# Kernel tuning notes

Hardware: AMD Instinct MI355X
Metric: run time of the kernel (lower is better)

Reference implementation:

```python
import jax, jax.numpy as jnp
import numpy as np

N_STEPS = 2
MAX_STEP = 1.0
EPS64 = float(np.finfo(np.float64).eps)


def _sphere_log(p, q):
    # log map on unit sphere, tangent at p pointing to q; p,q: [..., D]
    cos = jnp.clip(jnp.sum(p * q, axis=-1, keepdims=True), -1.0, 1.0)
    u = q - cos * p
    un = jnp.linalg.norm(u, axis=-1, keepdims=True)
    theta = jnp.arccos(cos)
    return theta * u / (un + 1e-12)


def _sphere_exp(p, v):
    # exp map on unit sphere; jnp.sinc(n/pi) = sin(n)/n (stable at 0)
    n = jnp.linalg.norm(v, axis=-1, keepdims=True)
    x = jnp.cos(n) * p + jnp.sinc(n / jnp.pi) * v
    return x / jnp.linalg.norm(x, axis=-1, keepdims=True)


def setup_inputs() -> dict:
    key = jax.random.key(0)
    ks = jax.random.split(key, 6)
    N, C, D, E = 50000, 16, 3, 1600000
    nodes = jax.random.normal(ks[0], (N, C, D), dtype=jnp.float32)
    nodes = nodes / jnp.linalg.norm(nodes, axis=-1, keepdims=True)  # points on S^2
    edge_w = jax.random.uniform(ks[1], (E,), dtype=jnp.float32)
    senders = jax.random.randint(ks[2], (E,), 0, N, dtype=jnp.int32)
    receivers = jax.random.randint(ks[3], (E,), 0, N, dtype=jnp.int32)
    t_sqrt = 1.0 + 0.3 * jax.random.normal(ks[4], (C,), dtype=jnp.float32)
    delta_sqrt = 1.0 + 0.3 * jax.random.normal(ks[5], (C,), dtype=jnp.float32)
    return {"nodes": nodes, "edge_w": edge_w, "t_sqrt": t_sqrt,
            "delta_sqrt": delta_sqrt, "senders": senders, "receivers": receivers}


def reference(nodes, edge_w, t_sqrt, delta_sqrt, senders, receivers):
    N = nodes.shape[0]
    t = (t_sqrt ** 2) / N_STEPS            # per-channel time, split across Euler steps
    delta = delta_sqrt ** 2                 # per-channel min step size
    deg = jax.ops.segment_sum(edge_w, senders, num_segments=N)  # [N]

    def laplace(x):
        # graph Laplacian of manifold-valued signal: weighted mean of log maps, negated
        logs = _sphere_log(x[senders], x[receivers])              # [E, C, D]
        agg = jax.ops.segment_sum(edge_w[:, None, None] * logs, senders, num_segments=N)
        return -agg / (deg[:, None, None] + 1e-12)                # [N, C, D]

    def step(x, _):
        v = laplace(x)
        nrm = jnp.sqrt(jnp.sum(v * v, axis=-1) + EPS64)           # [N, C]
        alp = jax.nn.sigmoid(nrm - delta[None, :])
        scale = jnp.where(nrm * alp <= MAX_STEP, alp, MAX_STEP / nrm)
        v = -(v * scale[..., None]) * t[None, :, None]
        return _sphere_exp(x, v), None

    x, _ = jax.lax.scan(step, nodes, None, length=N_STEPS, unroll=N_STEPS)
    return x
```

## Files before the change

kernel.cpp:

```cpp
#include <hip/hip_runtime.h>
#include <math.h>


constexpr float EPS64F = 2.2204460492503131e-16f;
constexpr float PI_F   = 3.14159265358979323846f;
constexpr int   SR_BITS = 14;
constexpr int   CH_BITS = 15;

typedef int   vi4 __attribute__((ext_vector_type(4)));
typedef float vf4 __attribute__((ext_vector_type(4)));
typedef float vf2 __attribute__((ext_vector_type(2)));


__global__ __launch_bounds__(256) void lhist_kernel(
    const int* __restrict__ snd, unsigned char* __restrict__ pos,
    unsigned char* __restrict__ partial2, int E, int NC) {
  __shared__ int h[1 << SR_BITS];
  int tid = threadIdx.x;
  int c = blockIdx.x, s = blockIdx.y;
  for (int i = tid; i < (1 << SR_BITS); i += 256) h[i] = 0;
  __syncthreads();
  int base = c << CH_BITS;
  int cnt = min(1 << CH_BITS, E - base);
  int s0 = s << SR_BITS;
  const vi4* snd4 = (const vi4*)(snd + base);
  int cnt4 = cnt >> 2;
  for (int i = tid; i < cnt4; i += 256) {
    vi4 sv = snd4[i];
    int e = base + (i << 2);
    int v;
    v = sv.x - s0; if ((unsigned)v < (1u << SR_BITS)) pos[e]     = (unsigned char)atomicAdd(&h[v], 1);
    v = sv.y - s0; if ((unsigned)v < (1u << SR_BITS)) pos[e + 1] = (unsigned char)atomicAdd(&h[v], 1);
    v = sv.z - s0; if ((unsigned)v < (1u << SR_BITS)) pos[e + 2] = (unsigned char)atomicAdd(&h[v], 1);
    v = sv.w - s0; if ((unsigned)v < (1u << SR_BITS)) pos[e + 3] = (unsigned char)atomicAdd(&h[v], 1);
  }
  if (tid == 0) {
    for (int i = cnt4 << 2; i < cnt; ++i) {
      int v = snd[base + i] - s0;
      if ((unsigned)v < (1u << SR_BITS))
        pos[base + i] = (unsigned char)atomicAdd(&h[v], 1);
    }
  }
  __syncthreads();
  unsigned char* dst = partial2 + ((size_t)(s * NC + c) << SR_BITS);
  for (int i = tid; i < (1 << SR_BITS); i += 256)
    dst[i] = (unsigned char)h[i];
}

__global__ __launch_bounds__(1024) void scan1A_kernel(
    const unsigned char* __restrict__ partial2, unsigned char* __restrict__ boffL,
    int* __restrict__ row_start, int* __restrict__ btot, int N, int NC) {
  __shared__ int wsum[16];
  int tid = threadIdx.x;
  int lane = tid & 63, wave = tid >> 6;
  int i = blockIdx.x * 1024 + tid;
  int vpad = 0;
  if (i < N) {
    int s = i >> SR_BITS, lv = i & ((1 << SR_BITS) - 1);
    int run = 0;
    for (int c = 0; c < NC; ++c) {
      int t = partial2[((size_t)(s * NC + c) << SR_BITS) + lv];
      boffL[(size_t)c * N + i] = (unsigned char)run;
      run += t;
    }
    vpad = (run + 15) & ~15;
  }
  int incl = vpad;
  #pragma unroll
  for (int off = 1; off < 64; off <<= 1) {
    int t = __shfl_up(incl, off, 64);
    if (lane >= off) incl += t;
  }
  if (lane == 63) wsum[wave] = incl;
  __syncthreads();
  if (wave == 0 && lane < 16) {
    int wincl = wsum[lane];
    #pragma unroll
    for (int off = 1; off < 16; off <<= 1) {
      int t = __shfl_up(wincl, off, 64);
      if (lane >= off) wincl += t;
    }
    wsum[lane] = wincl;
  }
  __syncthreads();
  int woff = (wave > 0) ? wsum[wave - 1] : 0;
  if (i < N) row_start[i] = woff + incl - vpad;
  if (tid == 0) btot[blockIdx.x] = wsum[15];
}

__global__ __launch_bounds__(256) void scanCD_kernel(
    int* __restrict__ row_start, const int* __restrict__ btot, int N, int nb) {
  __shared__ int bsh[64];
  int tid = threadIdx.x;
  if (tid < 64) {
    int v = (tid < nb) ? btot[tid] : 0;
    int incl = v;
    #pragma unroll
    for (int off = 1; off < 64; off <<= 1) {
      int t = __shfl_up(incl, off, 64);
      if (tid >= off) incl += t;
    }
    bsh[tid] = incl - v;
    if (blockIdx.x == 0 && tid == 63) row_start[N] = incl;
  }
  __syncthreads();
  int i = blockIdx.x * 256 + tid;
  if (i >= N) return;
  row_start[i] = row_start[i] + bsh[i >> 10];
}

__global__ __launch_bounds__(256) void fill_kernel(
    const vi4* __restrict__ snd4, const vi4* __restrict__ rcv4,
    const vf4* __restrict__ ew4, const unsigned char* __restrict__ pos,
    const unsigned char* __restrict__ boffL, const int* __restrict__ row_start,
    long long* __restrict__ pair,
    const int* __restrict__ snd, const int* __restrict__ rcv,
    const float* __restrict__ ew, int N, int E) {
  int tid = threadIdx.x;
  int E4 = E >> 2;
  #pragma unroll
  for (int gg = 0; gg < 2; ++gg) {
    int g = blockIdx.x * 512 + gg * 256 + tid;
    if (g < E4) {
      int e = g << 2;
      const unsigned char* bc = boffL + (size_t)(e >> CH_BITS) * N;
      vi4 s = __builtin_nontemporal_load(&snd4[g]);
      vi4 r = __builtin_nontemporal_load(&rcv4[g]);
      vf4 w = __builtin_nontemporal_load(&ew4[g]);
      unsigned pb = *(const unsigned*)(pos + e);
      int rs0 = row_start[s.x] + bc[s.x];
      int rs1 = row_start[s.y] + bc[s.y];
      int rs2 = row_start[s.z] + bc[s.z];
      int rs3 = row_start[s.w] + bc[s.w];
      pair[rs0 + (pb & 255u)] =
          (long long)(((unsigned long long)(unsigned)__float_as_int(w.x) << 32) | (unsigned)(r.x * 48));
      pair[rs1 + ((pb >> 8) & 255u)] =
          (long long)(((unsigned long long)(unsigned)__float_as_int(w.y) << 32) | (unsigned)(r.y * 48));
      pair[rs2 + ((pb >> 16) & 255u)] =
          (long long)(((unsigned long long)(unsigned)__float_as_int(w.z) << 32) | (unsigned)(r.z * 48));
      pair[rs3 + (pb >> 24)] =
          (long long)(((unsigned long long)(unsigned)__float_as_int(w.w) << 32) | (unsigned)(r.w * 48));
    }
  }
  if (blockIdx.x == 0 && tid == 0) {
    for (int e = E4 << 2; e < E; ++e) {
      int sn = snd[e];
      pair[row_start[sn] + boffL[(size_t)(e >> CH_BITS) * N + sn] + pos[e]] =
          (long long)(((unsigned long long)(unsigned)__float_as_int(ew[e]) << 32) | (unsigned)(rcv[e] * 48));
    }
  }
}


__device__ __forceinline__ void edge_accum_pk(
    vf2 p0, vf2 p1, vf2 p2, vf2 q0, vf2 q1, vf2 q2, vf2 w,
    vf2& a0, vf2& a1, vf2& a2) {
  vf2 cs = p0 * q0 + p1 * q1 + p2 * q2;
  cs = __builtin_elementwise_min(vf2{1.f, 1.f},
       __builtin_elementwise_max(vf2{-1.f, -1.f}, cs));
  vf2 u0 = q0 - cs * p0;
  vf2 u1 = q1 - cs * p1;
  vf2 u2 = q2 - cs * p2;
  vf2 un2 = __builtin_elementwise_max(u0 * u0 + u1 * u1 + u2 * u2,
                                      vf2{1e-24f, 1e-24f});
  vf2 ax = __builtin_elementwise_abs(cs);
  vf2 s = __builtin_elementwise_sqrt(vf2{1.f, 1.f} - ax);
  vf2 poly = ((ax * -0.0187293f + 0.0742610f) * ax - 0.2121144f) * ax
             + 1.5707288f;
  vf2 th = s * poly;
  vf2 theta;
  theta.x = (cs.x >= 0.0f) ? th.x : (PI_F - th.x);
  theta.y = (cs.y >= 0.0f) ? th.y : (PI_F - th.y);
  vf2 rsq;
  rsq.x = __builtin_amdgcn_rsqf(un2.x);
  rsq.y = __builtin_amdgcn_rsqf(un2.y);
  vf2 coef = w * theta * rsq;
  a0 += coef * u0;
  a1 += coef * u1;
  a2 += coef * u2;
}

__device__ __forceinline__ void node_step(
    float a0, float a1, float a2, float ws, float p0, float p1, float p2,
    float ts, float dsv, float& y0, float& y1, float& y2) {
  float invdg = __builtin_amdgcn_rcpf(ws + 1e-12f);
  float g0 = a0 * invdg, g1 = a1 * invdg, g2 = a2 * invdg;
  float nrm = sqrtf(fmaf(g0, g0, fmaf(g1, g1, g2 * g2)) + EPS64F);
  float tch = ts * ts * 0.5f;
  float dch = dsv * dsv;
  float alp = __builtin_amdgcn_rcpf(1.0f + __expf(dch - nrm));
  float scale = (nrm * alp <= 1.0f) ? alp : __builtin_amdgcn_rcpf(nrm);
  float f = scale * tch;
  float v0 = g0 * f, v1 = g1 * f, v2 = g2 * f;
  float nv = sqrtf(fmaf(v0, v0, fmaf(v1, v1, v2 * v2)));
  float cn = __cosf(nv);
  float sc = (nv > 1e-20f) ? (__sinf(nv) * __builtin_amdgcn_rcpf(nv)) : 1.0f;
  float t0 = fmaf(cn, p0, sc * v0);
  float t1 = fmaf(cn, p1, sc * v1);
  float t2 = fmaf(cn, p2, sc * v2);
  float inv = __builtin_amdgcn_rsqf(fmaf(t0, t0, fmaf(t1, t1, t2 * t2)));
  y0 = t0 * inv; y1 = t1 * inv; y2 = t2 * inv;
}

__global__ __launch_bounds__(256, 6) void flowp_kernel(
    const float* __restrict__ xin, const int* __restrict__ row_start,
    const long long* __restrict__ pair, const float* __restrict__ tsq,
    const float* __restrict__ dsq, float* __restrict__ xout, int N) {
  int node = blockIdx.x * 4 + (threadIdx.x >> 6);
  if (node >= N) return;
  int lane = threadIdx.x & 63;
  int c = lane & 15;
  int k = lane >> 4;
  int c3 = c * 3;
  int beg = row_start[node];
  int end = row_start[node + 1];
  int ip = node * 48 + c3;
  float ps0 = xin[ip], ps1 = xin[ip + 1], ps2 = xin[ip + 2];
  vf2 p0 = {ps0, ps0}, p1 = {ps1, ps1}, p2 = {ps2, ps2};
  vf2 a0 = {0.f, 0.f}, a1 = {0.f, 0.f}, a2 = {0.f, 0.f}, wsv = {0.f, 0.f};
  int iters = (end - beg) >> 4;
  if (iters > 0) {
    int j = beg + k;
    long long t0 = __builtin_nontemporal_load(&pair[j]);
    long long t1 = __builtin_nontemporal_load(&pair[j + 4]);
    long long t2 = __builtin_nontemporal_load(&pair[j + 8]);
    long long t3 = __builtin_nontemporal_load(&pair[j + 12]);
    long long eb0 = __builtin_nontemporal_load(&pair[j + 16]);
    long long eb1 = __builtin_nontemporal_load(&pair[j + 20]);
    long long eb2 = __builtin_nontemporal_load(&pair[j + 24]);
    long long eb3 = __builtin_nontemporal_load(&pair[j + 28]);
    float w0 = __int_as_float((int)(t0 >> 32));
    float w1 = __int_as_float((int)(t1 >> 32));
    float w2 = __int_as_float((int)(t2 >> 32));
    float w3 = __int_as_float((int)(t3 >> 32));
    const float* qp;
    qp = xin + ((int)t0 + c3); float qa0 = qp[0], qa1 = qp[1], qa2 = qp[2];
    qp = xin + ((int)t1 + c3); float qb0 = qp[0], qb1 = qp[1], qb2 = qp[2];
    qp = xin + ((int)t2 + c3); float qc0 = qp[0], qc1 = qp[1], qc2 = qp[2];
    qp = xin + ((int)t3 + c3); float qd0 = qp[0], qd1 = qp[1], qd2 = qp[2];
    #pragma unroll 2
    for (int t = 0; t < iters; ++t, j += 16) {
      long long ec0 = __builtin_nontemporal_load(&pair[j + 32]);
      long long ec1 = __builtin_nontemporal_load(&pair[j + 36]);
      long long ec2 = __builtin_nontemporal_load(&pair[j + 40]);
      long long ec3 = __builtin_nontemporal_load(&pair[j + 44]);
      float nw0 = __int_as_float((int)(eb0 >> 32));
      float nw1 = __int_as_float((int)(eb1 >> 32));
      float nw2 = __int_as_float((int)(eb2 >> 32));
      float nw3 = __int_as_float((int)(eb3 >> 32));
      const float* np;
      np = xin + ((int)eb0 + c3); float na0 = np[0], na1 = np[1], na2 = np[2];
      np = xin + ((int)eb1 + c3); float nb0 = np[0], nb1 = np[1], nb2 = np[2];
      np = xin + ((int)eb2 + c3); float nc0 = np[0], nc1 = np[1], nc2 = np[2];
      np = xin + ((int)eb3 + c3); float nd0 = np[0], nd1 = np[1], nd2 = np[2];
      vf2 wA = {w0, w1}, wB = {w2, w3};
      edge_accum_pk(p0, p1, p2, vf2{qa0, qb0}, vf2{qa1, qb1},
                    vf2{qa2, qb2}, wA, a0, a1, a2);
      edge_accum_pk(p0, p1, p2, vf2{qc0, qd0}, vf2{qc1, qd1},
                    vf2{qc2, qd2}, wB, a0, a1, a2);
      wsv += wA + wB;
      w0 = nw0; w1 = nw1; w2 = nw2; w3 = nw3;
      qa0 = na0; qa1 = na1; qa2 = na2;
      qb0 = nb0; qb1 = nb1; qb2 = nb2;
      qc0 = nc0; qc1 = nc1; qc2 = nc2;
      qd0 = nd0; qd1 = nd1; qd2 = nd2;
      eb0 = ec0; eb1 = ec1; eb2 = ec2; eb3 = ec3;
    }
  }
  float A0 = a0.x + a0.y, A1 = a1.x + a1.y, A2 = a2.x + a2.y;
  float ws = wsv.x + wsv.y;
  A0 += __shfl_xor(A0, 16); A1 += __shfl_xor(A1, 16);
  A2 += __shfl_xor(A2, 16); ws += __shfl_xor(ws, 16);
  A0 += __shfl_xor(A0, 32); A1 += __shfl_xor(A1, 32);
  A2 += __shfl_xor(A2, 32); ws += __shfl_xor(ws, 32);
  if (k == 0) {
    float y0, y1, y2;
    node_step(A0, A1, A2, ws, ps0, ps1, ps2, tsq[c], dsq[c], y0, y1, y2);
    xout[ip] = y0; xout[ip + 1] = y1; xout[ip + 2] = y2;
  }
}

static inline size_t al16(size_t x) { return (x + 15) & ~(size_t)15; }

extern "C" void kernel_launch(void* const* d_in, const int* in_sizes, int n_in,
                              void* d_out, int out_size, void* d_ws, size_t ws_size,
                              hipStream_t stream) {
  const float* nodes = (const float*)d_in[0];
  const float* ew    = (const float*)d_in[1];
  const float* tsq   = (const float*)d_in[2];
  const float* dsq   = (const float*)d_in[3];
  const int*   snd   = (const int*)d_in[4];
  const int*   rcv   = (const int*)d_in[5];
  float* out = (float*)d_out;

  int E = in_sizes[1];
  int N = in_sizes[0] / 48;

  int NS = (N + (1 << SR_BITS) - 1) >> SR_BITS;
  int NC = (E + (1 << CH_BITS) - 1) >> CH_BITS;

  size_t padN  = (size_t)E + 15 * (size_t)N + 64;
  size_t rsB   = al16((size_t)(N + 4) * 4);
  size_t auxB  = 512;
  size_t pairB = al16(padN * 8);
  size_t p2B   = al16((size_t)NS * NC << SR_BITS);
  size_t boffB = al16((size_t)NC * N * 4);

  char* base = (char*)d_ws;
  int*           row_start = (int*)base;
  int*           btot      = (int*)(base + rsB);
  long long*     pair      = (long long*)(base + rsB + auxB);
  unsigned char* partial2  = (unsigned char*)(base + rsB + auxB + pairB);
  unsigned char* boffL     = (unsigned char*)(base + rsB + auxB + pairB + p2B);
  unsigned char* pos       = (unsigned char*)(base + rsB + auxB + pairB + p2B + boffB);
  float*         xtmp      = (float*)boffL;

  int E4  = E >> 2;
  int nb  = (N + 1023) / 1024;
  int nb2 = (N + 255) / 256;
  int fbk = (E4 + 511) / 512;
  int nfb = (N + 3) / 4;

  hipMemsetAsync(pair, 0, pairB, stream);
  lhist_kernel<<<dim3(NC, NS), 256, 0, stream>>>(snd, pos, partial2, E, NC);
  scan1A_kernel<<<nb, 1024, 0, stream>>>(partial2, boffL, row_start, btot, N, NC);
  scanCD_kernel<<<nb2, 256, 0, stream>>>(row_start, btot, N, nb);
  fill_kernel<<<fbk, 256, 0, stream>>>((const vi4*)snd, (const vi4*)rcv,
                                       (const vf4*)ew, pos, boffL, row_start,
                                       pair, snd, rcv, ew, N, E);

  flowp_kernel<<<nfb, 256, 0, stream>>>(nodes, row_start, pair, tsq, dsq, xtmp, N);
  flowp_kernel<<<nfb, 256, 0, stream>>>(xtmp, row_start, pair, tsq, dsq, out, N);
}
```

Before: 275.4 us.

## Gather neighbor positions in fp16 and simplify edge loop with higher occupancy

A half-precision copy of the node positions is built inside the scan kernel. Both Euler-step kernels now gather neighbour coordinates from fp16 arrays, and the first step writes its intermediate result in fp16, which halves the bytes of the random gathers that dominate the flow kernels. The centre point for the first step is still read in fp32, but the second step reads its centre from the fp16 intermediate. The hand-written register prefetch pipeline is removed in favour of a plain loop, and the occupancy hint is raised from 6 to 8 to hide latency instead. This trades accuracy (fp16 rounding on the log-map inputs) for less memory traffic.

```diff
diff --git a/kernel.cpp b/kernel.cpp
--- a/kernel.cpp
+++ b/kernel.cpp
@@ -7,9 +7,10 @@
 constexpr int   SR_BITS = 14;
 constexpr int   CH_BITS = 15;
 
-typedef int   vi4 __attribute__((ext_vector_type(4)));
-typedef float vf4 __attribute__((ext_vector_type(4)));
-typedef float vf2 __attribute__((ext_vector_type(2)));
+typedef int      vi4 __attribute__((ext_vector_type(4)));
+typedef float    vf4 __attribute__((ext_vector_type(4)));
+typedef float    vf2 __attribute__((ext_vector_type(2)));
+typedef _Float16 vh4 __attribute__((ext_vector_type(4)));
 
 
 __global__ __launch_bounds__(256) void lhist_kernel(
@@ -89,7 +90,9 @@
 }
 
 __global__ __launch_bounds__(256) void scanCD_kernel(
-    int* __restrict__ row_start, const int* __restrict__ btot, int N, int nb) {
+    int* __restrict__ row_start, const int* __restrict__ btot,
+    const vf4* __restrict__ nodes4, _Float16* __restrict__ nodes_h,
+    int N, int nb) {
   __shared__ int bsh[64];
   int tid = threadIdx.x;
   if (tid < 64) {
@@ -105,8 +108,13 @@
   }
   __syncthreads();
   int i = blockIdx.x * 256 + tid;
-  if (i >= N) return;
-  row_start[i] = row_start[i] + bsh[i >> 10];
+  if (i < N) row_start[i] = row_start[i] + bsh[i >> 10];
+  int total = N * 12;
+  for (int idx = blockIdx.x * 256 + tid; idx < total; idx += gridDim.x * 256) {
+    vf4 v = nodes4[idx];
+    vh4 h = {(_Float16)v.x, (_Float16)v.y, (_Float16)v.z, (_Float16)v.w};
+    ((vh4*)nodes_h)[idx] = h;
+  }
 }
 
 __global__ __launch_bounds__(256) void fill_kernel(
@@ -202,10 +210,11 @@
   y0 = t0 * inv; y1 = t1 * inv; y2 = t2 * inv;
 }
 
-__global__ __launch_bounds__(256, 6) void flowp_kernel(
-    const float* __restrict__ xin, const int* __restrict__ row_start,
-    const long long* __restrict__ pair, const float* __restrict__ tsq,
-    const float* __restrict__ dsq, float* __restrict__ xout, int N) {
+__global__ __launch_bounds__(256, 8) void flowp_kernel(
+    const _Float16* __restrict__ xh, const float* __restrict__ pf,
+    const int* __restrict__ row_start, const long long* __restrict__ pair,
+    const float* __restrict__ tsq, const float* __restrict__ dsq,
+    float* __restrict__ of, _Float16* __restrict__ oh, int N) {
   int node = blockIdx.x * 4 + (threadIdx.x >> 6);
   if (node >= N) return;
   int lane = threadIdx.x & 63;
@@ -215,57 +224,36 @@
   int beg = row_start[node];
   int end = row_start[node + 1];
   int ip = node * 48 + c3;
-  float ps0 = xin[ip], ps1 = xin[ip + 1], ps2 = xin[ip + 2];
+  float ps0, ps1, ps2;
+  if (pf) {
+    ps0 = pf[ip]; ps1 = pf[ip + 1]; ps2 = pf[ip + 2];
+  } else {
+    ps0 = (float)xh[ip]; ps1 = (float)xh[ip + 1]; ps2 = (float)xh[ip + 2];
+  }
   vf2 p0 = {ps0, ps0}, p1 = {ps1, ps1}, p2 = {ps2, ps2};
   vf2 a0 = {0.f, 0.f}, a1 = {0.f, 0.f}, a2 = {0.f, 0.f}, wsv = {0.f, 0.f};
   int iters = (end - beg) >> 4;
-  if (iters > 0) {
-    int j = beg + k;
-    long long t0 = __builtin_nontemporal_load(&pair[j]);
-    long long t1 = __builtin_nontemporal_load(&pair[j + 4]);
-    long long t2 = __builtin_nontemporal_load(&pair[j + 8]);
-    long long t3 = __builtin_nontemporal_load(&pair[j + 12]);
-    long long eb0 = __builtin_nontemporal_load(&pair[j + 16]);
-    long long eb1 = __builtin_nontemporal_load(&pair[j + 20]);
-    long long eb2 = __builtin_nontemporal_load(&pair[j + 24]);
-    long long eb3 = __builtin_nontemporal_load(&pair[j + 28]);
-    float w0 = __int_as_float((int)(t0 >> 32));
-    float w1 = __int_as_float((int)(t1 >> 32));
-    float w2 = __int_as_float((int)(t2 >> 32));
-    float w3 = __int_as_float((int)(t3 >> 32));
-    const float* qp;
-    qp = xin + ((int)t0 + c3); float qa0 = qp[0], qa1 = qp[1], qa2 = qp[2];
-    qp = xin + ((int)t1 + c3); float qb0 = qp[0], qb1 = qp[1], qb2 = qp[2];
-    qp = xin + ((int)t2 + c3); float qc0 = qp[0], qc1 = qp[1], qc2 = qp[2];
-    qp = xin + ((int)t3 + c3); float qd0 = qp[0], qd1 = qp[1], qd2 = qp[2];
-    #pragma unroll 2
-    for (int t = 0; t < iters; ++t, j += 16) {
-      long long ec0 = __builtin_nontemporal_load(&pair[j + 32]);
-      long long ec1 = __builtin_nontemporal_load(&pair[j + 36]);
-      long long ec2 = __builtin_nontemporal_load(&pair[j + 40]);
-      long long ec3 = __builtin_nontemporal_load(&pair[j + 44]);
-      float nw0 = __int_as_float((int)(eb0 >> 32));
-      float nw1 = __int_as_float((int)(eb1 >> 32));
-      float nw2 = __int_as_float((int)(eb2 >> 32));
-      float nw3 = __int_as_float((int)(eb3 >> 32));
-      const float* np;
-      np = xin + ((int)eb0 + c3); float na0 = np[0], na1 = np[1], na2 = np[2];
-      np = xin + ((int)eb1 + c3); float nb0 = np[0], nb1 = np[1], nb2 = np[2];
-      np = xin + ((int)eb2 + c3); float nc0 = np[0], nc1 = np[1], nc2 = np[2];
-      np = xin + ((int)eb3 + c3); float nd0 = np[0], nd1 = np[1], nd2 = np[2];
-      vf2 wA = {w0, w1}, wB = {w2, w3};
-      edge_accum_pk(p0, p1, p2, vf2{qa0, qb0}, vf2{qa1, qb1},
-                    vf2{qa2, qb2}, wA, a0, a1, a2);
-      edge_accum_pk(p0, p1, p2, vf2{qc0, qd0}, vf2{qc1, qd1},
-                    vf2{qc2, qd2}, wB, a0, a1, a2);
-      wsv += wA + wB;
-      w0 = nw0; w1 = nw1; w2 = nw2; w3 = nw3;
-      qa0 = na0; qa1 = na1; qa2 = na2;
-      qb0 = nb0; qb1 = nb1; qb2 = nb2;
-      qc0 = nc0; qc1 = nc1; qc2 = nc2;
-      qd0 = nd0; qd1 = nd1; qd2 = nd2;
-      eb0 = ec0; eb1 = ec1; eb2 = ec2; eb3 = ec3;
-    }
+  int j = beg + k;
+  for (int t = 0; t < iters; ++t, j += 16) {
+    long long e0 = __builtin_nontemporal_load(&pair[j]);
+    long long e1 = __builtin_nontemporal_load(&pair[j + 4]);
+    long long e2 = __builtin_nontemporal_load(&pair[j + 8]);
+    long long e3 = __builtin_nontemporal_load(&pair[j + 12]);
+    float w0 = __int_as_float((int)(e0 >> 32));
+    float w1 = __int_as_float((int)(e1 >> 32));
+    float w2 = __int_as_float((int)(e2 >> 32));
+    float w3 = __int_as_float((int)(e3 >> 32));
+    const _Float16* qp;
+    qp = xh + ((int)e0 + c3); float qa0 = qp[0], qa1 = qp[1], qa2 = qp[2];
+    qp = xh + ((int)e1 + c3); float qb0 = qp[0], qb1 = qp[1], qb2 = qp[2];
+    qp = xh + ((int)e2 + c3); float qc0 = qp[0], qc1 = qp[1], qc2 = qp[2];
+    qp = xh + ((int)e3 + c3); float qd0 = qp[0], qd1 = qp[1], qd2 = qp[2];
+    vf2 wA = {w0, w1}, wB = {w2, w3};
+    edge_accum_pk(p0, p1, p2, vf2{qa0, qb0}, vf2{qa1, qb1},
+                  vf2{qa2, qb2}, wA, a0, a1, a2);
+    edge_accum_pk(p0, p1, p2, vf2{qc0, qd0}, vf2{qc1, qd1},
+                  vf2{qc2, qd2}, wB, a0, a1, a2);
+    wsv += wA + wB;
   }
   float A0 = a0.x + a0.y, A1 = a1.x + a1.y, A2 = a2.x + a2.y;
   float ws = wsv.x + wsv.y;
@@ -276,7 +264,12 @@
   if (k == 0) {
     float y0, y1, y2;
     node_step(A0, A1, A2, ws, ps0, ps1, ps2, tsq[c], dsq[c], y0, y1, y2);
-    xout[ip] = y0; xout[ip + 1] = y1; xout[ip + 2] = y2;
+    if (of) { of[ip] = y0; of[ip + 1] = y1; of[ip + 2] = y2; }
+    if (oh) {
+      oh[ip]     = (_Float16)y0;
+      oh[ip + 1] = (_Float16)y1;
+      oh[ip + 2] = (_Float16)y2;
+    }
   }
 }
 
@@ -304,7 +297,9 @@
   size_t auxB  = 512;
   size_t pairB = al16(padN * 8);
   size_t p2B   = al16((size_t)NS * NC << SR_BITS);
+  size_t xhB   = al16((size_t)N * 96);
   size_t boffB = al16((size_t)NC * N * 4);
+  if (boffB < 2 * xhB) boffB = 2 * xhB;
 
   char* base = (char*)d_ws;
   int*           row_start = (int*)base;
@@ -313,7 +308,8 @@
   unsigned char* partial2  = (unsigned char*)(base + rsB + auxB + pairB);
   unsigned char* boffL     = (unsigned char*)(base + rsB + auxB + pairB + p2B);
   unsigned char* pos       = (unsigned char*)(base + rsB + auxB + pairB + p2B + boffB);
-  float*         xtmp      = (float*)boffL;
+  _Float16*      xtmp_h    = (_Float16*)boffL;
+  _Float16*      nodes_h   = (_Float16*)((char*)boffL + xhB);
 
   int E4  = E >> 2;
   int nb  = (N + 1023) / 1024;
@@ -324,11 +320,14 @@
   hipMemsetAsync(pair, 0, pairB, stream);
   lhist_kernel<<<dim3(NC, NS), 256, 0, stream>>>(snd, pos, partial2, E, NC);
   scan1A_kernel<<<nb, 1024, 0, stream>>>(partial2, boffL, row_start, btot, N, NC);
-  scanCD_kernel<<<nb2, 256, 0, stream>>>(row_start, btot, N, nb);
+  scanCD_kernel<<<nb2, 256, 0, stream>>>(row_start, btot, (const vf4*)nodes,
+                                         nodes_h, N, nb);
   fill_kernel<<<fbk, 256, 0, stream>>>((const vi4*)snd, (const vi4*)rcv,
                                        (const vf4*)ew, pos, boffL, row_start,
                                        pair, snd, rcv, ew, N, E);
 
-  flowp_kernel<<<nfb, 256, 0, stream>>>(nodes, row_start, pair, tsq, dsq, xtmp, N);
-  flowp_kernel<<<nfb, 256, 0, stream>>>(xtmp, row_start, pair, tsq, dsq, out, N);
-}
+  flowp_kernel<<<nfb, 256, 0, stream>>>(nodes_h, nodes, row_start, pair,
+                                        tsq, dsq, nullptr, xtmp_h, N);
+  flowp_kernel<<<nfb, 256, 0, stream>>>(xtmp_h, nullptr, row_start, pair,
+                                        tsq, dsq, out, nullptr, N);
+}
```

Result: slower. 303.9 us (+10.3%).
